# Optimization experiments

Hardware: AMD Instinct MI355X
Metric: run time of the kernel (lower is better)

## Reference

```python
import jax, jax.numpy as jnp
import numpy as np


def _conv1x1(x, w, b):
    # x: [B,C,H,W], w: [O,C], b: [O] -> [B,O,H,W]
    return jnp.einsum('bchw,oc->bohw', x, w) + b[None, :, None, None]


def setup_inputs() -> dict:
    key = jax.random.key(0)
    ks = jax.random.split(key, 11)
    B, C, Ci, H, W = 4, 256, 128, 64, 64
    s_in = 1.0 / np.sqrt(C)
    s_ci = 1.0 / np.sqrt(Ci)
    return {
        'x': jax.random.normal(ks[0], (B, C, H, W), jnp.float32),
        'g_w': jax.random.normal(ks[1], (Ci, C), jnp.float32) * s_in,
        'g_b': jax.random.normal(ks[2], (Ci,), jnp.float32) * 0.01,
        'theta_w': jax.random.normal(ks[3], (Ci, C), jnp.float32) * s_in,
        'theta_b': jax.random.normal(ks[4], (Ci,), jnp.float32) * 0.01,
        'phi_w': jax.random.normal(ks[5], (Ci, C), jnp.float32) * s_in,
        'phi_b': jax.random.normal(ks[6], (Ci,), jnp.float32) * 0.01,
        'wz_w': jax.random.normal(ks[7], (C, Ci), jnp.float32) * s_ci,
        'wz_b': jax.random.normal(ks[8], (C,), jnp.float32) * 0.01,
        'bn_gamma': jax.random.uniform(ks[9], (C,), jnp.float32, 0.5, 1.5),
        'bn_beta': jax.random.normal(ks[10], (C,), jnp.float32) * 0.01,
    }


def reference(x, g_w, g_b, theta_w, theta_b, phi_w, phi_b, wz_w, wz_b, bn_gamma, bn_beta):
    B, C, H, W = x.shape
    Ci = g_w.shape[0]
    N = H * W
    # 1x1 conv projections, flattened over spatial positions
    g_x = _conv1x1(x, g_w, g_b).reshape(B, Ci, N).transpose(0, 2, 1)       # [B,N,Ci]
    theta_x = _conv1x1(x, theta_w, theta_b).reshape(B, Ci, N)              # [B,Ci,N]
    phi_x = _conv1x1(x, phi_w, phi_b).reshape(B, Ci, N)                    # [B,Ci,N]
    # f[b, i, j] = theta_i . phi_j  -> [B,N,N]
    f = jnp.einsum('bci,bcj->bij', theta_x, phi_x)
    # NOTE: softmax over dim=1 (query axis) — faithful to original (non-standard)
    f_div_C = jax.nn.softmax(f, axis=1)
    y = jnp.einsum('bij,bjc->bic', f_div_C, g_x)                           # [B,N,Ci]
    y = y.transpose(0, 2, 1).reshape(B, Ci, H, W)                          # [B,Ci,H,W]
    # W_z: 1x1 conv + BatchNorm2d (training-mode batch statistics)
    w_y = _conv1x1(y, wz_w, wz_b)                                          # [B,C,H,W]
    mean = jnp.mean(w_y, axis=(0, 2, 3), keepdims=True)
    var = jnp.var(w_y, axis=(0, 2, 3), keepdims=True)
    w_y = (w_y - mean) * jax.lax.rsqrt(var + 1e-5)
    w_y = w_y * bn_gamma[None, :, None, None] + bn_beta[None, :, None, None]
    return w_y + x
```

## Files before the change

### kernel.cpp

```cpp
#include <hip/hip_runtime.h>


#define B_  4
#define C_  256
#define CI  128
#define N_  4096
#define NB  (B_*N_)
#define ISPLIT 16
#define MB_ (1u<<20)
#define LOG2E 1.442695041f

typedef _Float16 f16;
typedef f16   f16x8 __attribute__((ext_vector_type(8)));
typedef f16   f16x4 __attribute__((ext_vector_type(4)));
typedef float f32x4 __attribute__((ext_vector_type(4)));
typedef float f32x16 __attribute__((ext_vector_type(16)));
typedef unsigned u32x2 __attribute__((ext_vector_type(2)));
typedef unsigned u32x4v __attribute__((ext_vector_type(4)));

#define MFMA(a,b,c)   __builtin_amdgcn_mfma_f32_16x16x32_f16(a,b,c,0,0,0)
#define MFMA32(a,b,c) __builtin_amdgcn_mfma_f32_32x32x16_f16(a,b,c,0,0,0)

#define GLD16(g, lp) __builtin_amdgcn_global_load_lds( \
    (const __attribute__((address_space(1))) void*)(g), \
    (__attribute__((address_space(3))) void*)(lp), 16, 0, 0)

#define OFF_THETA  0
#define OFF_PHI    (4u*MB_)
#define OFF_G      (8u*MB_)
#define OFF_YP     (12u*MB_)
#define OFF_WY     0
#define OFF_PS     (28u*MB_)
#define OFF_PSUM   OFF_PS
#define OFF_WCVT   (OFF_PS + ISPLIT*NB*4)
#define PSZ ((size_t)B_*N_*CI)

__global__ void k_init(const float* gw, const float* tw, const float* pw,
                       const float* zw, f16* wcvt) {
    int i = blockIdx.x * 256 + threadIdx.x;
    const float* s;
    int which = i >> 15;
    if (which == 0) s = gw; else if (which == 1) s = tw;
    else if (which == 2) s = pw; else s = zw;
    wcvt[i] = (f16)s[i & 32767];
}

__global__ __launch_bounds__(256) void k_proj(
        const float* __restrict__ x, const f16* __restrict__ wcvt,
        const float* __restrict__ gb, const float* __restrict__ tb,
        const float* __restrict__ pb,
        f16* __restrict__ thetaT, f16* __restrict__ phiT, f16* __restrict__ gC) {
    __shared__ __align__(16) f16 xT[32 * 264];
    int bb = blockIdx.x >> 7;
    int n0 = (blockIdx.x & 127) * 32;
    int t = threadIdx.x;

    const float* xb = x + (size_t)bb * C_ * N_;
    for (int rep = 0; rep < 8; rep++) {
        int lin = rep * 256 + t;
        int c = lin >> 3, np = (lin & 7) * 4;
        float4 v = *reinterpret_cast<const float4*>(xb + c * N_ + n0 + np);
        xT[(np + 0) * 264 + c] = (f16)v.x;
        xT[(np + 1) * 264 + c] = (f16)v.y;
        xT[(np + 2) * 264 + c] = (f16)v.z;
        xT[(np + 3) * 264 + c] = (f16)v.w;
    }
    __syncthreads();

    int w = t >> 6, l16 = t & 15, q = (t & 63) >> 4;
    int ci0 = w * 32;
    for (int proj = 0; proj < 3; proj++) {
        const f16* W0 = wcvt + proj * 32768;
        f32x4 acc[2][2] = {};
        for (int kk = 0; kk < 8; kk++) {
            f16x8 a0 = *reinterpret_cast<const f16x8*>(W0 + (ci0 + l16) * 256 + kk * 32 + q * 8);
            f16x8 a1 = *reinterpret_cast<const f16x8*>(W0 + (ci0 + 16 + l16) * 256 + kk * 32 + q * 8);
#pragma unroll
            for (int nt = 0; nt < 2; nt++) {
                f16x8 bv = *reinterpret_cast<const f16x8*>(&xT[(nt * 16 + l16) * 264 + kk * 32 + q * 8]);
                acc[0][nt] = MFMA(a0, bv, acc[0][nt]);
                acc[1][nt] = MFMA(a1, bv, acc[1][nt]);
            }
        }
        const float* bias = (proj == 0) ? gb : (proj == 1) ? tb : pb;
        float scl = (proj == 1) ? LOG2E : 1.0f;
#pragma unroll
        for (int a = 0; a < 2; a++) {
#pragma unroll
            for (int nt = 0; nt < 2; nt++) {
                int n = n0 + nt * 16 + l16;
                int cib = ci0 + a * 16 + q * 4;
                if (proj == 0) {
#pragma unroll
                    for (int r = 0; r < 4; r++)
                        gC[((size_t)bb * CI + cib + r) * N_ + n] = (f16)(acc[a][nt][r] + bias[cib + r]);
                } else {
                    f16x4 v4;
#pragma unroll
                    for (int r = 0; r < 4; r++)
                        v4[r] = (f16)((acc[a][nt][r] + bias[cib + r]) * scl);
                    f16* dst = (proj == 1 ? thetaT : phiT) + ((size_t)bb * N_ + n) * CI + cib;
                    *reinterpret_cast<f16x4*>(dst) = v4;
                }
            }
        }
    }
}

__global__ __launch_bounds__(256, 4) void k_cols(
        const f16* __restrict__ thetaT, const f16* __restrict__ phiT,
        float* __restrict__ ps) {
    __shared__ __align__(16) f16 thS[2][64 * 128];
    int id = blockIdx.x;
    int isp = id & 15, jb = (id >> 4) & 31, bb = id >> 9;
    int t = threadIdx.x, w = t >> 6, l = t & 63;
    int l31 = l & 31, hi = l >> 5;
    int jw = jb * 128 + w * 32 + l31;

    f16x8 pf[8];
    const f16* pb = phiT + ((size_t)bb * N_ + jw) * CI + hi * 8;
#pragma unroll
    for (int kk = 0; kk < 8; kk++)
        pf[kk] = *reinterpret_cast<const f16x8*>(pb + kk * 16);

    const f16* thB = thetaT + ((size_t)bb * N_ + isp * 256) * CI;
    auto stage = [&](int bf, int it0) {
#pragma unroll
        for (int r = 0; r < 4; r++) {
            int p = r * 256 + w * 64 + l;
            int pi = p >> 4, pu = (p & 15) ^ (pi & 15);
            const char* ga = (const char*)(thB + (size_t)(it0 + pi) * CI) + pu * 16;
            GLD16(ga, &thS[bf][(r * 256 + w * 64) * 8]);
        }
    };

    float s = 0.f;
    stage(0, 0);
    __syncthreads();
    for (int it = 0; it < 4; it++) {
        int bf = it & 1;
        if (it + 1 < 4) stage(bf ^ 1, (it + 1) * 64);
#pragma unroll
        for (int it2 = 0; it2 < 2; it2++) {
            f16x8 av[8];
#pragma unroll
            for (int kk = 0; kk < 8; kk++)
                av[kk] = *reinterpret_cast<const f16x8*>(
                    &thS[bf][(it2 * 32 + l31) * 128 + (((kk * 2 + hi) ^ (l31 & 15)) * 8)]);
            f32x16 f = {};
            __builtin_amdgcn_s_setprio(1);
#pragma unroll
            for (int kk = 0; kk < 8; kk++)
                f = MFMA32(av[kk], pf[kk], f);
            __builtin_amdgcn_s_setprio(0);
#pragma unroll
            for (int r = 0; r < 16; r++)
                s += __builtin_amdgcn_exp2f(f[r]);
        }
        __syncthreads();
    }
    s += __shfl_xor(s, 32);
    if (hi == 0)
        ps[isp * NB + bb * N_ + jw] = s;
}

__global__ __launch_bounds__(512, 2) void k_attn(
        const f16* __restrict__ thetaT, const f16* __restrict__ phiT,
        const f16* __restrict__ gC, const float* __restrict__ ps,
        f16* __restrict__ yP) {
    __shared__ __align__(16) char smem[102400];
    f16 (*phiS)[64 * 128] = (f16(*)[64 * 128])smem;
    f16 (*gS)[128 * 64]   = (f16(*)[128 * 64])(smem + 49152);
    float* mdL = (float*)(smem + 98304);

    int jq = blockIdx.x & 3;
    int ib = blockIdx.x >> 2;
    int bb = ib >> 4;
    int i0 = (ib & 15) * 256;
    int t = threadIdx.x, w = t >> 6, l = t & 63;
    int l31 = l & 31, hi = l >> 5;
    int js = w >> 2, iw = w & 3;
    int jbase = jq * 1024;

    {
        const float* pp = ps + bb * N_ + jbase;
        float s0 = 0.f, s1 = 0.f;
#pragma unroll
        for (int isp = 0; isp < ISPLIT; isp++) {
            s0 += pp[isp * NB + t];
            s1 += pp[isp * NB + t + 512];
        }
        mdL[t]       = -__log2f(s0);
        mdL[t + 512] = -__log2f(s1);
    }

    f16x8 ta[2][8];
#pragma unroll
    for (int is = 0; is < 2; is++) {
        const f16* tb = thetaT + ((size_t)bb * N_ + i0 + iw * 64 + is * 32 + l31) * CI + hi * 8;
#pragma unroll
        for (int kk = 0; kk < 8; kk++)
            ta[is][kk] = *reinterpret_cast<const f16x8*>(tb + kk * 16);
    }

    const f16* phiB = phiT + (size_t)bb * N_ * CI;
    const f16* gB   = gC   + (size_t)bb * CI * N_;

    auto stage = [&](int bf, int j0g) {
#pragma unroll
        for (int r = 0; r < 2; r++) {
            int p = r * 512 + t;
            int ub = (r * 512 + w * 64) * 8;
            int pj = p >> 4, pu = (p & 15) ^ (pj & 15);
            const char* ga = (const char*)(phiB + (size_t)(j0g + pj) * CI) + pu * 16;
            GLD16(ga, &phiS[bf][ub]);
            int pc = p >> 3, pu2 = (p & 7) ^ (pc & 7);
            const char* ga2 = (const char*)(gB + (size_t)pc * N_ + j0g) + pu2 * 16;
            GLD16(ga2, &gS[bf][ub]);
        }
    };

    stage(0, jbase);
    stage(1, jbase + 64);
    asm volatile("s_waitcnt vmcnt(4) lgkmcnt(0)" ::: "memory");
    __builtin_amdgcn_s_barrier();

    f32x16 yacc[2][4] = {};
    for (int jt = 0; jt < 16; jt++) {
        int bf = jt % 3;
        if (jt + 2 < 16) stage((jt + 2) % 3, jbase + (jt + 2) * 64);

        f32x16 facc[2];
#pragma unroll
        for (int c = 0; c < 4; c++) {
            f32x4 v = *reinterpret_cast<const f32x4*>(
                &mdL[jt * 64 + js * 32 + c * 8 + hi * 4]);
            facc[0][c * 4 + 0] = v[0]; facc[0][c * 4 + 1] = v[1];
            facc[0][c * 4 + 2] = v[2]; facc[0][c * 4 + 3] = v[3];
            facc[1][c * 4 + 0] = v[0]; facc[1][c * 4 + 1] = v[1];
            facc[1][c * 4 + 2] = v[2]; facc[1][c * 4 + 3] = v[3];
        }

        __builtin_amdgcn_s_setprio(1);
#pragma unroll
        for (int kk = 0; kk < 8; kk++) {
            f16x8 pv = *reinterpret_cast<const f16x8*>(
                &phiS[bf][(js * 32 + l31) * 128 + (((kk * 2 + hi) ^ (l31 & 15)) * 8)]);
            facc[0] = MFMA32(pv, ta[0][kk], facc[0]);
            facc[1] = MFMA32(pv, ta[1][kk], facc[1]);
        }
        __builtin_amdgcn_s_setprio(0);

#pragma unroll
        for (int ch = 0; ch < 2; ch++) {
            f16x8 wfr[2];
#pragma unroll
            for (int is = 0; is < 2; is++) {
                float e0 = __builtin_amdgcn_exp2f(facc[is][ch * 8 + 0]);
                float e1 = __builtin_amdgcn_exp2f(facc[is][ch * 8 + 1]);
                float e2 = __builtin_amdgcn_exp2f(facc[is][ch * 8 + 2]);
                float e3 = __builtin_amdgcn_exp2f(facc[is][ch * 8 + 3]);
                float e4 = __builtin_amdgcn_exp2f(facc[is][ch * 8 + 4]);
                float e5 = __builtin_amdgcn_exp2f(facc[is][ch * 8 + 5]);
                float e6 = __builtin_amdgcn_exp2f(facc[is][ch * 8 + 6]);
                float e7 = __builtin_amdgcn_exp2f(facc[is][ch * 8 + 7]);
                unsigned p01 = __builtin_bit_cast(unsigned, __builtin_amdgcn_cvt_pkrtz(e0, e1));
                unsigned p23 = __builtin_bit_cast(unsigned, __builtin_amdgcn_cvt_pkrtz(e2, e3));
                unsigned p45 = __builtin_bit_cast(unsigned, __builtin_amdgcn_cvt_pkrtz(e4, e5));
                unsigned p67 = __builtin_bit_cast(unsigned, __builtin_amdgcn_cvt_pkrtz(e6, e7));
                u32x2 s0 = __builtin_amdgcn_permlane32_swap(p01, p45, false, false);
                u32x2 s1 = __builtin_amdgcn_permlane32_swap(p23, p67, false, false);
                u32x4v wu = {s0[0], s1[0], s0[1], s1[1]};
                wfr[is] = __builtin_bit_cast(f16x8, wu);
            }
            int jc = js * 2 + ch;
            __builtin_amdgcn_s_setprio(1);
#pragma unroll
            for (int cs = 0; cs < 4; cs++) {
                f16x8 gv = *reinterpret_cast<const f16x8*>(
                    &gS[bf][(cs * 32 + l31) * 64 + (((jc * 2 + hi) ^ (l31 & 7)) * 8)]);
                yacc[0][cs] = MFMA32(wfr[0], gv, yacc[0][cs]);
                yacc[1][cs] = MFMA32(wfr[1], gv, yacc[1][cs]);
            }
            __builtin_amdgcn_s_setprio(0);
        }

        if (jt < 14) { asm volatile("s_waitcnt vmcnt(4)" ::: "memory"); }
        else         { asm volatile("s_waitcnt vmcnt(0)" ::: "memory"); }
        __builtin_amdgcn_s_barrier();
    }

    float* red = (float*)smem;
#pragma unroll
    for (int is = 0; is < 2; is++) {
        __syncthreads();
        if (js == 1) {
#pragma unroll
            for (int cs = 0; cs < 4; cs++)
#pragma unroll
                for (int rq = 0; rq < 4; rq++) {
                    f32x4 v;
                    v[0] = yacc[is][cs][rq * 4 + 0];
                    v[1] = yacc[is][cs][rq * 4 + 1];
                    v[2] = yacc[is][cs][rq * 4 + 2];
                    v[3] = yacc[is][cs][rq * 4 + 3];
                    *reinterpret_cast<f32x4*>(&red[((iw * 4 + cs) * 4 + rq) * 256 + l * 4]) = v;
                }
        }
        __syncthreads();
        if (js == 0) {
#pragma unroll
            for (int cs = 0; cs < 4; cs++)
#pragma unroll
                for (int rq = 0; rq < 4; rq++) {
                    f32x4 v = *reinterpret_cast<const f32x4*>(
                        &red[((iw * 4 + cs) * 4 + rq) * 256 + l * 4]);
                    yacc[is][cs][rq * 4 + 0] += v[0];
                    yacc[is][cs][rq * 4 + 1] += v[1];
                    yacc[is][cs][rq * 4 + 2] += v[2];
                    yacc[is][cs][rq * 4 + 3] += v[3];
                }
        }
    }
    __syncthreads();

    if (js == 0) {
        f16* yw = (f16*)smem + iw * (32 * 136);
#pragma unroll
        for (int is = 0; is < 2; is++) {
#pragma unroll
            for (int cs = 0; cs < 4; cs++)
#pragma unroll
                for (int r = 0; r < 16; r++)
                    yw[((r & 3) + 8 * (r >> 2) + 4 * hi) * 136 + cs * 32 + l31] =
                        (f16)yacc[is][cs][r];
            f16* yo = yP + (size_t)jq * PSZ + ((size_t)bb * N_ + i0 + iw * 64 + is * 32) * CI;
            __builtin_amdgcn_s_waitcnt(0);
#pragma unroll
            for (int rr = 0; rr < 8; rr++) {
                int chunk = rr * 64 + l;
                int il = chunk >> 4, u = chunk & 15;
                *reinterpret_cast<f16x8*>(yo + il * CI + u * 8) =
                    *reinterpret_cast<const f16x8*>(&yw[il * 136 + u * 8]);
            }
            __builtin_amdgcn_s_waitcnt(0);
        }
    }
}

__global__ __launch_bounds__(256) void k_wz(
        const f16* __restrict__ wzc, const f16* __restrict__ yP,
        const float* __restrict__ zb, f16* __restrict__ wy,
        float* __restrict__ psum) {
    int id = blockIdx.x;
    int nb = id & 127, bb = id >> 7;
    int t = threadIdx.x, w = t >> 6, l16 = t & 15, q = (t & 63) >> 4;
    int o0 = w * 64, n0 = nb * 32;
    f32x4 acc[4][2] = {};
#pragma unroll
    for (int kk = 0; kk < 4; kk++) {
        f16x8 bv[2];
#pragma unroll
        for (int nt = 0; nt < 2; nt++) {
            size_t yi = ((size_t)bb * N_ + n0 + nt * 16 + l16) * CI + kk * 32 + q * 8;
            f16x8 b0 = *reinterpret_cast<const f16x8*>(yP + yi);
            f16x8 b1 = *reinterpret_cast<const f16x8*>(yP + PSZ + yi);
            f16x8 b2 = *reinterpret_cast<const f16x8*>(yP + 2 * PSZ + yi);
            f16x8 b3 = *reinterpret_cast<const f16x8*>(yP + 3 * PSZ + yi);
            bv[nt] = (b0 + b1) + (b2 + b3);
        }
#pragma unroll
        for (int os = 0; os < 4; os++) {
            f16x8 av = *reinterpret_cast<const f16x8*>(
                wzc + (o0 + os * 16 + l16) * CI + kk * 32 + q * 8);
#pragma unroll
            for (int nt = 0; nt < 2; nt++)
                acc[os][nt] = MFMA(av, bv[nt], acc[os][nt]);
        }
    }
#pragma unroll
    for (int os = 0; os < 4; os++)
#pragma unroll
    for (int r = 0; r < 4; r++) {
        int o = o0 + os * 16 + q * 4 + r;
        float bias = zb[o];
        float sr = 0.f, qr = 0.f;
#pragma unroll
        for (int nt = 0; nt < 2; nt++) {
            float v = acc[os][nt][r] + bias;
            wy[((size_t)bb * C_ + o) * N_ + n0 + nt * 16 + l16] = (f16)v;
            sr += v; qr += v * v;
        }
#pragma unroll
        for (int off = 1; off < 16; off <<= 1) {
            sr += __shfl_xor(sr, off);
            qr += __shfl_xor(qr, off);
        }
        if (l16 == 0) {
            psum[(o * 2 + 0) * 512 + id] = sr;
            psum[(o * 2 + 1) * 512 + id] = qr;
        }
    }
}

__global__ void k_final(const f16* __restrict__ wy, const float* __restrict__ x,
                        const float* __restrict__ psum,
                        const float* __restrict__ gamma, const float* __restrict__ beta,
                        float* __restrict__ out) {
    __shared__ float s8[8];
    int t = threadIdx.x;
    int p = blockIdx.x * 256 + t;
    int c = (p >> 9) & 255;
    float sr = psum[(c * 2 + 0) * 512 + t] + psum[(c * 2 + 0) * 512 + 256 + t];
    float qr = psum[(c * 2 + 1) * 512 + t] + psum[(c * 2 + 1) * 512 + 256 + t];
#pragma unroll
    for (int off = 1; off < 64; off <<= 1) {
        sr += __shfl_xor(sr, off);
        qr += __shfl_xor(qr, off);
    }
    int w = t >> 6;
    if ((t & 63) == 0) { s8[w * 2] = sr; s8[w * 2 + 1] = qr; }
    __syncthreads();
    float ssum = s8[0] + s8[2] + s8[4] + s8[6];
    float ssq  = s8[1] + s8[3] + s8[5] + s8[7];

    const float inv = 1.0f / 16384.0f;
    float mean = ssum * inv;
    float var = ssq * inv - mean * mean;
    float s = gamma[c] * rsqrtf(var + 1e-5f);
    float h = beta[c] - mean * s;
    f16x8 wv = reinterpret_cast<const f16x8*>(wy)[p];
    float4 x0 = reinterpret_cast<const float4*>(x)[2 * p];
    float4 x1 = reinterpret_cast<const float4*>(x)[2 * p + 1];
    float4 o0, o1;
    o0.x = (float)wv[0] * s + h + x0.x;
    o0.y = (float)wv[1] * s + h + x0.y;
    o0.z = (float)wv[2] * s + h + x0.z;
    o0.w = (float)wv[3] * s + h + x0.w;
    o1.x = (float)wv[4] * s + h + x1.x;
    o1.y = (float)wv[5] * s + h + x1.y;
    o1.z = (float)wv[6] * s + h + x1.z;
    o1.w = (float)wv[7] * s + h + x1.w;
    reinterpret_cast<float4*>(out)[2 * p] = o0;
    reinterpret_cast<float4*>(out)[2 * p + 1] = o1;
}

extern "C" void kernel_launch(void* const* d_in, const int* in_sizes, int n_in,
                              void* d_out, int out_size, void* d_ws, size_t ws_size,
                              hipStream_t stream) {
    const float* x     = (const float*)d_in[0];
    const float* gw    = (const float*)d_in[1];
    const float* gb    = (const float*)d_in[2];
    const float* tw    = (const float*)d_in[3];
    const float* tbv   = (const float*)d_in[4];
    const float* pw    = (const float*)d_in[5];
    const float* pb    = (const float*)d_in[6];
    const float* zw    = (const float*)d_in[7];
    const float* zb    = (const float*)d_in[8];
    const float* gamma = (const float*)d_in[9];
    const float* beta  = (const float*)d_in[10];

    char* ws = (char*)d_ws;
    f16* thetaT = (f16*)(ws + OFF_THETA);
    f16* phiT   = (f16*)(ws + OFF_PHI);
    f16* gC     = (f16*)(ws + OFF_G);
    f16* yP     = (f16*)(ws + OFF_YP);
    f16* wy     = (f16*)(ws + OFF_WY);
    f16* wcvt   = (f16*)(ws + OFF_WCVT);
    float* ps   = (float*)(ws + OFF_PS);
    float* psum = (float*)(ws + OFF_PSUM);

    k_init<<<512, 256, 0, stream>>>(gw, tw, pw, zw, wcvt);
    k_proj<<<512, 256, 0, stream>>>(x, wcvt, gb, tbv, pb, thetaT, phiT, gC);
    k_cols<<<2048, 256, 0, stream>>>(thetaT, phiT, ps);
    k_attn<<<256, 512, 0, stream>>>(thetaT, phiT, gC, ps, yP);
    k_wz<<<512, 256, 0, stream>>>(wcvt + 3 * 32768, yP, zb, wy, psum);
    k_final<<<2048, 256, 0, stream>>>(wy, x, psum, gamma, beta, (float*)d_out);
}
```

Baseline: 188.0 us.

## Fuse all six stages into one cooperative persistent kernel with grid syncs

Replaces the six separate kernel launches with one cooperative kernel of 256 blocks of 512 threads, which uses grid.sync between the weight conversion, projection, column-sum, attention, Wz and BatchNorm-final phases. Each block takes on two or more of the old blocks' work units per phase. The aim is to remove launch gaps and inter-kernel drain and fill overhead. In exchange, phases that previously used 2048 small blocks now run on a fixed grid with serial repetitions, and each grid barrier costs some time.

```diff
diff --git a/kernel.cpp b/kernel.cpp
--- a/kernel.cpp
+++ b/kernel.cpp
@@ -1,5 +1,8 @@
 #include <hip/hip_runtime.h>
-
+#include <hip/hip_cooperative_groups.h>
+
+
+namespace cg = cooperative_groups;
 
 #define B_  4
 #define C_  256
@@ -35,414 +38,437 @@
 #define OFF_WCVT   (OFF_PS + ISPLIT*NB*4)
 #define PSZ ((size_t)B_*N_*CI)
 
-__global__ void k_init(const float* gw, const float* tw, const float* pw,
-                       const float* zw, f16* wcvt) {
-    int i = blockIdx.x * 256 + threadIdx.x;
-    const float* s;
-    int which = i >> 15;
-    if (which == 0) s = gw; else if (which == 1) s = tw;
-    else if (which == 2) s = pw; else s = zw;
-    wcvt[i] = (f16)s[i & 32767];
-}
-
-__global__ __launch_bounds__(256) void k_proj(
-        const float* __restrict__ x, const f16* __restrict__ wcvt,
-        const float* __restrict__ gb, const float* __restrict__ tb,
-        const float* __restrict__ pb,
-        f16* __restrict__ thetaT, f16* __restrict__ phiT, f16* __restrict__ gC) {
-    __shared__ __align__(16) f16 xT[32 * 264];
-    int bb = blockIdx.x >> 7;
-    int n0 = (blockIdx.x & 127) * 32;
+__global__ __launch_bounds__(512, 2) void k_mono(
+        const float* __restrict__ x,
+        const float* __restrict__ gw, const float* __restrict__ gb,
+        const float* __restrict__ tw, const float* __restrict__ tbv,
+        const float* __restrict__ pw, const float* __restrict__ pb,
+        const float* __restrict__ zw, const float* __restrict__ zb,
+        const float* __restrict__ gamma, const float* __restrict__ beta,
+        float* __restrict__ out, char* __restrict__ ws) {
+    cg::grid_group grid = cg::this_grid();
+    __shared__ __align__(16) char smem[102400];
+
+    f16* thetaT = (f16*)(ws + OFF_THETA);
+    f16* phiT   = (f16*)(ws + OFF_PHI);
+    f16* gC     = (f16*)(ws + OFF_G);
+    f16* yP     = (f16*)(ws + OFF_YP);
+    f16* wy     = (f16*)(ws + OFF_WY);
+    f16* wcvt   = (f16*)(ws + OFF_WCVT);
+    float* ps   = (float*)(ws + OFF_PS);
+    float* psum = (float*)(ws + OFF_PSUM);
+
     int t = threadIdx.x;
-
-    const float* xb = x + (size_t)bb * C_ * N_;
-    for (int rep = 0; rep < 8; rep++) {
-        int lin = rep * 256 + t;
-        int c = lin >> 3, np = (lin & 7) * 4;
-        float4 v = *reinterpret_cast<const float4*>(xb + c * N_ + n0 + np);
-        xT[(np + 0) * 264 + c] = (f16)v.x;
-        xT[(np + 1) * 264 + c] = (f16)v.y;
-        xT[(np + 2) * 264 + c] = (f16)v.z;
-        xT[(np + 3) * 264 + c] = (f16)v.w;
-    }
-    __syncthreads();
-
-    int w = t >> 6, l16 = t & 15, q = (t & 63) >> 4;
-    int ci0 = w * 32;
-    for (int proj = 0; proj < 3; proj++) {
-        const f16* W0 = wcvt + proj * 32768;
-        f32x4 acc[2][2] = {};
-        for (int kk = 0; kk < 8; kk++) {
-            f16x8 a0 = *reinterpret_cast<const f16x8*>(W0 + (ci0 + l16) * 256 + kk * 32 + q * 8);
-            f16x8 a1 = *reinterpret_cast<const f16x8*>(W0 + (ci0 + 16 + l16) * 256 + kk * 32 + q * 8);
+    int blk = blockIdx.x;
+    int sub = t >> 8, tt = t & 255;
+
+    {
+        int i = blk * 512 + t;
+        const float* s;
+        int which = i >> 15;
+        if (which == 0) s = gw; else if (which == 1) s = tw;
+        else if (which == 2) s = pw; else s = zw;
+        wcvt[i] = (f16)s[i & 32767];
+    }
+    __threadfence();
+    grid.sync();
+
+    {
+        f16* xT = (f16*)smem + (size_t)sub * (32 * 264);
+        int vid = blk * 2 + sub;
+        int bb = vid >> 7;
+        int n0 = (vid & 127) * 32;
+
+        const float* xb = x + (size_t)bb * C_ * N_;
+        for (int rep = 0; rep < 8; rep++) {
+            int lin = rep * 256 + tt;
+            int c = lin >> 3, np = (lin & 7) * 4;
+            float4 v = *reinterpret_cast<const float4*>(xb + c * N_ + n0 + np);
+            xT[(np + 0) * 264 + c] = (f16)v.x;
+            xT[(np + 1) * 264 + c] = (f16)v.y;
+            xT[(np + 2) * 264 + c] = (f16)v.z;
+            xT[(np + 3) * 264 + c] = (f16)v.w;
+        }
+        __syncthreads();
+
+        int w4 = tt >> 6, l16 = tt & 15, q = (tt & 63) >> 4;
+        int ci0 = w4 * 32;
+        for (int proj = 0; proj < 3; proj++) {
+            const f16* W0 = wcvt + proj * 32768;
+            f32x4 acc[2][2] = {};
+            for (int kk = 0; kk < 8; kk++) {
+                f16x8 a0 = *reinterpret_cast<const f16x8*>(W0 + (ci0 + l16) * 256 + kk * 32 + q * 8);
+                f16x8 a1 = *reinterpret_cast<const f16x8*>(W0 + (ci0 + 16 + l16) * 256 + kk * 32 + q * 8);
+#pragma unroll
+                for (int nt = 0; nt < 2; nt++) {
+                    f16x8 bv = *reinterpret_cast<const f16x8*>(&xT[(nt * 16 + l16) * 264 + kk * 32 + q * 8]);
+                    acc[0][nt] = MFMA(a0, bv, acc[0][nt]);
+                    acc[1][nt] = MFMA(a1, bv, acc[1][nt]);
+                }
+            }
+            const float* bias = (proj == 0) ? gb : (proj == 1) ? tbv : pb;
+            float scl = (proj == 1) ? LOG2E : 1.0f;
+#pragma unroll
+            for (int a = 0; a < 2; a++) {
+#pragma unroll
+                for (int nt = 0; nt < 2; nt++) {
+                    int n = n0 + nt * 16 + l16;
+                    int cib = ci0 + a * 16 + q * 4;
+                    if (proj == 0) {
+#pragma unroll
+                        for (int r = 0; r < 4; r++)
+                            gC[((size_t)bb * CI + cib + r) * N_ + n] = (f16)(acc[a][nt][r] + bias[cib + r]);
+                    } else {
+                        f16x4 v4;
+#pragma unroll
+                        for (int r = 0; r < 4; r++)
+                            v4[r] = (f16)((acc[a][nt][r] + bias[cib + r]) * scl);
+                        f16* dst = (proj == 1 ? thetaT : phiT) + ((size_t)bb * N_ + n) * CI + cib;
+                        *reinterpret_cast<f16x4*>(dst) = v4;
+                    }
+                }
+            }
+        }
+    }
+    __threadfence();
+    grid.sync();
+
+    {
+        f16* thS = (f16*)smem + (size_t)sub * 16384;
+        int wl = tt >> 6, l = tt & 63, l31 = l & 31, hi = l >> 5;
+        for (int rep = 0; rep < 4; rep++) {
+            int unit = blk * 8 + sub * 4 + rep;
+            int isp = unit & 15, jb = (unit >> 4) & 31, bb = unit >> 9;
+            int jw = jb * 128 + wl * 32 + l31;
+
+            f16x8 pf[8];
+            const f16* pb2 = phiT + ((size_t)bb * N_ + jw) * CI + hi * 8;
+#pragma unroll
+            for (int kk = 0; kk < 8; kk++)
+                pf[kk] = *reinterpret_cast<const f16x8*>(pb2 + kk * 16);
+
+            const f16* thB = thetaT + ((size_t)bb * N_ + isp * 256) * CI;
+            auto stage = [&](int bf, int it0) {
+#pragma unroll
+                for (int r = 0; r < 4; r++) {
+                    int p = r * 256 + wl * 64 + l;
+                    int pi = p >> 4, pu = (p & 15) ^ (pi & 15);
+                    const char* ga = (const char*)(thB + (size_t)(it0 + pi) * CI) + pu * 16;
+                    GLD16(ga, thS + bf * 8192 + (r * 256 + wl * 64) * 8);
+                }
+            };
+
+            float s = 0.f;
+            stage(0, 0);
+            __syncthreads();
+            for (int it = 0; it < 4; it++) {
+                int bf = it & 1;
+                if (it + 1 < 4) stage(bf ^ 1, (it + 1) * 64);
+#pragma unroll
+                for (int it2 = 0; it2 < 2; it2++) {
+                    f16x8 av[8];
+#pragma unroll
+                    for (int kk = 0; kk < 8; kk++)
+                        av[kk] = *reinterpret_cast<const f16x8*>(
+                            thS + bf * 8192 + (it2 * 32 + l31) * 128 + (((kk * 2 + hi) ^ (l31 & 15)) * 8));
+                    f32x16 f = {};
+                    __builtin_amdgcn_s_setprio(1);
+#pragma unroll
+                    for (int kk = 0; kk < 8; kk++)
+                        f = MFMA32(av[kk], pf[kk], f);
+                    __builtin_amdgcn_s_setprio(0);
+#pragma unroll
+                    for (int r = 0; r < 16; r++)
+                        s += __builtin_amdgcn_exp2f(f[r]);
+                }
+                __syncthreads();
+            }
+            s += __shfl_xor(s, 32);
+            if (hi == 0)
+                ps[isp * NB + bb * N_ + jw] = s;
+        }
+    }
+    __threadfence();
+    grid.sync();
+
+    {
+        f16 (*phiS)[64 * 128] = (f16(*)[64 * 128])smem;
+        f16 (*gS)[128 * 64]   = (f16(*)[128 * 64])(smem + 49152);
+        float* mdL = (float*)(smem + 98304);
+
+        int jq = blk & 3;
+        int ib = blk >> 2;
+        int bb = ib >> 4;
+        int i0 = (ib & 15) * 256;
+        int w = t >> 6, l = t & 63;
+        int l31 = l & 31, hi = l >> 5;
+        int js = w >> 2, iw = w & 3;
+        int jbase = jq * 1024;
+
+        {
+            const float* pp = ps + bb * N_ + jbase;
+            float s0 = 0.f, s1 = 0.f;
+#pragma unroll
+            for (int isp = 0; isp < ISPLIT; isp++) {
+                s0 += pp[isp * NB + t];
+                s1 += pp[isp * NB + t + 512];
+            }
+            mdL[t]       = -__log2f(s0);
+            mdL[t + 512] = -__log2f(s1);
+        }
+
+        f16x8 ta[2][8];
+#pragma unroll
+        for (int is = 0; is < 2; is++) {
+            const f16* tb = thetaT + ((size_t)bb * N_ + i0 + iw * 64 + is * 32 + l31) * CI + hi * 8;
+#pragma unroll
+            for (int kk = 0; kk < 8; kk++)
+                ta[is][kk] = *reinterpret_cast<const f16x8*>(tb + kk * 16);
+        }
+
+        const f16* phiB = phiT + (size_t)bb * N_ * CI;
+        const f16* gB   = gC   + (size_t)bb * CI * N_;
+
+        auto stage = [&](int bf, int j0g) {
+#pragma unroll
+            for (int r = 0; r < 2; r++) {
+                int p = r * 512 + t;
+                int ub = (r * 512 + w * 64) * 8;
+                int pj = p >> 4, pu = (p & 15) ^ (pj & 15);
+                const char* ga = (const char*)(phiB + (size_t)(j0g + pj) * CI) + pu * 16;
+                GLD16(ga, &phiS[bf][ub]);
+                int pc = p >> 3, pu2 = (p & 7) ^ (pc & 7);
+                const char* ga2 = (const char*)(gB + (size_t)pc * N_ + j0g) + pu2 * 16;
+                GLD16(ga2, &gS[bf][ub]);
+            }
+        };
+
+        stage(0, jbase);
+        stage(1, jbase + 64);
+        asm volatile("s_waitcnt vmcnt(4) lgkmcnt(0)" ::: "memory");
+        __builtin_amdgcn_s_barrier();
+
+        f32x16 yacc[2][4] = {};
+        for (int jt = 0; jt < 16; jt++) {
+            int bf = jt % 3;
+            if (jt + 2 < 16) stage((jt + 2) % 3, jbase + (jt + 2) * 64);
+
+            f32x16 facc[2];
+#pragma unroll
+            for (int c = 0; c < 4; c++) {
+                f32x4 v = *reinterpret_cast<const f32x4*>(
+                    &mdL[jt * 64 + js * 32 + c * 8 + hi * 4]);
+                facc[0][c * 4 + 0] = v[0]; facc[0][c * 4 + 1] = v[1];
+                facc[0][c * 4 + 2] = v[2]; facc[0][c * 4 + 3] = v[3];
+                facc[1][c * 4 + 0] = v[0]; facc[1][c * 4 + 1] = v[1];
+                facc[1][c * 4 + 2] = v[2]; facc[1][c * 4 + 3] = v[3];
+            }
+
+            __builtin_amdgcn_s_setprio(1);
+#pragma unroll
+            for (int kk = 0; kk < 8; kk++) {
+                f16x8 pv = *reinterpret_cast<const f16x8*>(
+                    &phiS[bf][(js * 32 + l31) * 128 + (((kk * 2 + hi) ^ (l31 & 15)) * 8)]);
+                facc[0] = MFMA32(pv, ta[0][kk], facc[0]);
+                facc[1] = MFMA32(pv, ta[1][kk], facc[1]);
+            }
+            __builtin_amdgcn_s_setprio(0);
+
+#pragma unroll
+            for (int ch = 0; ch < 2; ch++) {
+                f16x8 wfr[2];
+#pragma unroll
+                for (int is = 0; is < 2; is++) {
+                    float e0 = __builtin_amdgcn_exp2f(facc[is][ch * 8 + 0]);
+                    float e1 = __builtin_amdgcn_exp2f(facc[is][ch * 8 + 1]);
+                    float e2 = __builtin_amdgcn_exp2f(facc[is][ch * 8 + 2]);
+                    float e3 = __builtin_amdgcn_exp2f(facc[is][ch * 8 + 3]);
+                    float e4 = __builtin_amdgcn_exp2f(facc[is][ch * 8 + 4]);
+                    float e5 = __builtin_amdgcn_exp2f(facc[is][ch * 8 + 5]);
+                    float e6 = __builtin_amdgcn_exp2f(facc[is][ch * 8 + 6]);
+                    float e7 = __builtin_amdgcn_exp2f(facc[is][ch * 8 + 7]);
+                    unsigned p01 = __builtin_bit_cast(unsigned, __builtin_amdgcn_cvt_pkrtz(e0, e1));
+                    unsigned p23 = __builtin_bit_cast(unsigned, __builtin_amdgcn_cvt_pkrtz(e2, e3));
+                    unsigned p45 = __builtin_bit_cast(unsigned, __builtin_amdgcn_cvt_pkrtz(e4, e5));
+                    unsigned p67 = __builtin_bit_cast(unsigned, __builtin_amdgcn_cvt_pkrtz(e6, e7));
+                    u32x2 s0 = __builtin_amdgcn_permlane32_swap(p01, p45, false, false);
+                    u32x2 s1 = __builtin_amdgcn_permlane32_swap(p23, p67, false, false);
+                    u32x4v wu = {s0[0], s1[0], s0[1], s1[1]};
+                    wfr[is] = __builtin_bit_cast(f16x8, wu);
+                }
+                int jc = js * 2 + ch;
+                __builtin_amdgcn_s_setprio(1);
+#pragma unroll
+                for (int cs = 0; cs < 4; cs++) {
+                    f16x8 gv = *reinterpret_cast<const f16x8*>(
+                        &gS[bf][(cs * 32 + l31) * 64 + (((jc * 2 + hi) ^ (l31 & 7)) * 8)]);
+                    yacc[0][cs] = MFMA32(wfr[0], gv, yacc[0][cs]);
+                    yacc[1][cs] = MFMA32(wfr[1], gv, yacc[1][cs]);
+                }
+                __builtin_amdgcn_s_setprio(0);
+            }
+
+            if (jt < 14) { asm volatile("s_waitcnt vmcnt(4)" ::: "memory"); }
+            else         { asm volatile("s_waitcnt vmcnt(0)" ::: "memory"); }
+            __builtin_amdgcn_s_barrier();
+        }
+
+        float* red = (float*)smem;
+#pragma unroll
+        for (int is = 0; is < 2; is++) {
+            __syncthreads();
+            if (js == 1) {
+#pragma unroll
+                for (int cs = 0; cs < 4; cs++)
+#pragma unroll
+                    for (int rq = 0; rq < 4; rq++) {
+                        f32x4 v;
+                        v[0] = yacc[is][cs][rq * 4 + 0];
+                        v[1] = yacc[is][cs][rq * 4 + 1];
+                        v[2] = yacc[is][cs][rq * 4 + 2];
+                        v[3] = yacc[is][cs][rq * 4 + 3];
+                        *reinterpret_cast<f32x4*>(&red[((iw * 4 + cs) * 4 + rq) * 256 + l * 4]) = v;
+                    }
+            }
+            __syncthreads();
+            if (js == 0) {
+#pragma unroll
+                for (int cs = 0; cs < 4; cs++)
+#pragma unroll
+                    for (int rq = 0; rq < 4; rq++) {
+                        f32x4 v = *reinterpret_cast<const f32x4*>(
+                            &red[((iw * 4 + cs) * 4 + rq) * 256 + l * 4]);
+                        yacc[is][cs][rq * 4 + 0] += v[0];
+                        yacc[is][cs][rq * 4 + 1] += v[1];
+                        yacc[is][cs][rq * 4 + 2] += v[2];
+                        yacc[is][cs][rq * 4 + 3] += v[3];
+                    }
+            }
+        }
+        __syncthreads();
+
+        if (js == 0) {
+            f16* yw = (f16*)smem + iw * (32 * 136);
+#pragma unroll
+            for (int is = 0; is < 2; is++) {
+#pragma unroll
+                for (int cs = 0; cs < 4; cs++)
+#pragma unroll
+                    for (int r = 0; r < 16; r++)
+                        yw[((r & 3) + 8 * (r >> 2) + 4 * hi) * 136 + cs * 32 + l31] =
+                            (f16)yacc[is][cs][r];
+                f16* yo = yP + (size_t)jq * PSZ + ((size_t)bb * N_ + i0 + iw * 64 + is * 32) * CI;
+                __builtin_amdgcn_s_waitcnt(0);
+#pragma unroll
+                for (int rr = 0; rr < 8; rr++) {
+                    int chunk = rr * 64 + l;
+                    int il = chunk >> 4, u = chunk & 15;
+                    *reinterpret_cast<f16x8*>(yo + il * CI + u * 8) =
+                        *reinterpret_cast<const f16x8*>(&yw[il * 136 + u * 8]);
+                }
+                __builtin_amdgcn_s_waitcnt(0);
+            }
+        }
+    }
+    __threadfence();
+    grid.sync();
+
+    {
+        const f16* wzc = wcvt + 3 * 32768;
+        int id = blk * 2 + sub;
+        int nb = id & 127, bb = id >> 7;
+        int w4 = tt >> 6, l16 = tt & 15, q = (tt & 63) >> 4;
+        int o0 = w4 * 64, n0 = nb * 32;
+        f32x4 acc[4][2] = {};
+#pragma unroll
+        for (int kk = 0; kk < 4; kk++) {
+            f16x8 bv[2];
 #pragma unroll
             for (int nt = 0; nt < 2; nt++) {
-                f16x8 bv = *reinterpret_cast<const f16x8*>(&xT[(nt * 16 + l16) * 264 + kk * 32 + q * 8]);
-                acc[0][nt] = MFMA(a0, bv, acc[0][nt]);
-                acc[1][nt] = MFMA(a1, bv, acc[1][nt]);
-            }
-        }
-        const float* bias = (proj == 0) ? gb : (proj == 1) ? tb : pb;
-        float scl = (proj == 1) ? LOG2E : 1.0f;
-#pragma unroll
-        for (int a = 0; a < 2; a++) {
+                size_t yi = ((size_t)bb * N_ + n0 + nt * 16 + l16) * CI + kk * 32 + q * 8;
+                f16x8 b0 = *reinterpret_cast<const f16x8*>(yP + yi);
+                f16x8 b1 = *reinterpret_cast<const f16x8*>(yP + PSZ + yi);
+                f16x8 b2 = *reinterpret_cast<const f16x8*>(yP + 2 * PSZ + yi);
+                f16x8 b3 = *reinterpret_cast<const f16x8*>(yP + 3 * PSZ + yi);
+                bv[nt] = (b0 + b1) + (b2 + b3);
+            }
+#pragma unroll
+            for (int os = 0; os < 4; os++) {
+                f16x8 av = *reinterpret_cast<const f16x8*>(
+                    wzc + (o0 + os * 16 + l16) * CI + kk * 32 + q * 8);
+#pragma unroll
+                for (int nt = 0; nt < 2; nt++)
+                    acc[os][nt] = MFMA(av, bv[nt], acc[os][nt]);
+            }
+        }
+#pragma unroll
+        for (int os = 0; os < 4; os++)
+#pragma unroll
+        for (int r = 0; r < 4; r++) {
+            int o = o0 + os * 16 + q * 4 + r;
+            float bias = zb[o];
+            float sr = 0.f, qr = 0.f;
 #pragma unroll
             for (int nt = 0; nt < 2; nt++) {
-                int n = n0 + nt * 16 + l16;
-                int cib = ci0 + a * 16 + q * 4;
-                if (proj == 0) {
-#pragma unroll
-                    for (int r = 0; r < 4; r++)
-                        gC[((size_t)bb * CI + cib + r) * N_ + n] = (f16)(acc[a][nt][r] + bias[cib + r]);
-                } else {
-                    f16x4 v4;
-#pragma unroll
-                    for (int r = 0; r < 4; r++)
-                        v4[r] = (f16)((acc[a][nt][r] + bias[cib + r]) * scl);
-                    f16* dst = (proj == 1 ? thetaT : phiT) + ((size_t)bb * N_ + n) * CI + cib;
-                    *reinterpret_cast<f16x4*>(dst) = v4;
-                }
-            }
-        }
-    }
-}
-
-__global__ __launch_bounds__(256, 4) void k_cols(
-        const f16* __restrict__ thetaT, const f16* __restrict__ phiT,
-        float* __restrict__ ps) {
-    __shared__ __align__(16) f16 thS[2][64 * 128];
-    int id = blockIdx.x;
-    int isp = id & 15, jb = (id >> 4) & 31, bb = id >> 9;
-    int t = threadIdx.x, w = t >> 6, l = t & 63;
-    int l31 = l & 31, hi = l >> 5;
-    int jw = jb * 128 + w * 32 + l31;
-
-    f16x8 pf[8];
-    const f16* pb = phiT + ((size_t)bb * N_ + jw) * CI + hi * 8;
-#pragma unroll
-    for (int kk = 0; kk < 8; kk++)
-        pf[kk] = *reinterpret_cast<const f16x8*>(pb + kk * 16);
-
-    const f16* thB = thetaT + ((size_t)bb * N_ + isp * 256) * CI;
-    auto stage = [&](int bf, int it0) {
-#pragma unroll
-        for (int r = 0; r < 4; r++) {
-            int p = r * 256 + w * 64 + l;
-            int pi = p >> 4, pu = (p & 15) ^ (pi & 15);
-            const char* ga = (const char*)(thB + (size_t)(it0 + pi) * CI) + pu * 16;
-            GLD16(ga, &thS[bf][(r * 256 + w * 64) * 8]);
-        }
-    };
-
-    float s = 0.f;
-    stage(0, 0);
-    __syncthreads();
-    for (int it = 0; it < 4; it++) {
-        int bf = it & 1;
-        if (it + 1 < 4) stage(bf ^ 1, (it + 1) * 64);
-#pragma unroll
-        for (int it2 = 0; it2 < 2; it2++) {
-            f16x8 av[8];
-#pragma unroll
-            for (int kk = 0; kk < 8; kk++)
-                av[kk] = *reinterpret_cast<const f16x8*>(
-                    &thS[bf][(it2 * 32 + l31) * 128 + (((kk * 2 + hi) ^ (l31 & 15)) * 8)]);
-            f32x16 f = {};
-            __builtin_amdgcn_s_setprio(1);
-#pragma unroll
-            for (int kk = 0; kk < 8; kk++)
-                f = MFMA32(av[kk], pf[kk], f);
-            __builtin_amdgcn_s_setprio(0);
-#pragma unroll
-            for (int r = 0; r < 16; r++)
-                s += __builtin_amdgcn_exp2f(f[r]);
-        }
-        __syncthreads();
-    }
-    s += __shfl_xor(s, 32);
-    if (hi == 0)
-        ps[isp * NB + bb * N_ + jw] = s;
-}
-
-__global__ __launch_bounds__(512, 2) void k_attn(
-        const f16* __restrict__ thetaT, const f16* __restrict__ phiT,
-        const f16* __restrict__ gC, const float* __restrict__ ps,
-        f16* __restrict__ yP) {
-    __shared__ __align__(16) char smem[102400];
-    f16 (*phiS)[64 * 128] = (f16(*)[64 * 128])smem;
-    f16 (*gS)[128 * 64]   = (f16(*)[128 * 64])(smem + 49152);
-    float* mdL = (float*)(smem + 98304);
-
-    int jq = blockIdx.x & 3;
-    int ib = blockIdx.x >> 2;
-    int bb = ib >> 4;
-    int i0 = (ib & 15) * 256;
-    int t = threadIdx.x, w = t >> 6, l = t & 63;
-    int l31 = l & 31, hi = l >> 5;
-    int js = w >> 2, iw = w & 3;
-    int jbase = jq * 1024;
-
-    {
-        const float* pp = ps + bb * N_ + jbase;
-        float s0 = 0.f, s1 = 0.f;
-#pragma unroll
-        for (int isp = 0; isp < ISPLIT; isp++) {
-            s0 += pp[isp * NB + t];
-            s1 += pp[isp * NB + t + 512];
-        }
-        mdL[t]       = -__log2f(s0);
-        mdL[t + 512] = -__log2f(s1);
-    }
-
-    f16x8 ta[2][8];
-#pragma unroll
-    for (int is = 0; is < 2; is++) {
-        const f16* tb = thetaT + ((size_t)bb * N_ + i0 + iw * 64 + is * 32 + l31) * CI + hi * 8;
-#pragma unroll
-        for (int kk = 0; kk < 8; kk++)
-            ta[is][kk] = *reinterpret_cast<const f16x8*>(tb + kk * 16);
-    }
-
-    const f16* phiB = phiT + (size_t)bb * N_ * CI;
-    const f16* gB   = gC   + (size_t)bb * CI * N_;
-
-    auto stage = [&](int bf, int j0g) {
-#pragma unroll
-        for (int r = 0; r < 2; r++) {
-            int p = r * 512 + t;
-            int ub = (r * 512 + w * 64) * 8;
-            int pj = p >> 4, pu = (p & 15) ^ (pj & 15);
-            const char* ga = (const char*)(phiB + (size_t)(j0g + pj) * CI) + pu * 16;
-            GLD16(ga, &phiS[bf][ub]);
-            int pc = p >> 3, pu2 = (p & 7) ^ (pc & 7);
-            const char* ga2 = (const char*)(gB + (size_t)pc * N_ + j0g) + pu2 * 16;
-            GLD16(ga2, &gS[bf][ub]);
-        }
-    };
-
-    stage(0, jbase);
-    stage(1, jbase + 64);
-    asm volatile("s_waitcnt vmcnt(4) lgkmcnt(0)" ::: "memory");
-    __builtin_amdgcn_s_barrier();
-
-    f32x16 yacc[2][4] = {};
-    for (int jt = 0; jt < 16; jt++) {
-        int bf = jt % 3;
-        if (jt + 2 < 16) stage((jt + 2) % 3, jbase + (jt + 2) * 64);
-
-        f32x16 facc[2];
-#pragma unroll
-        for (int c = 0; c < 4; c++) {
-            f32x4 v = *reinterpret_cast<const f32x4*>(
-                &mdL[jt * 64 + js * 32 + c * 8 + hi * 4]);
-            facc[0][c * 4 + 0] = v[0]; facc[0][c * 4 + 1] = v[1];
-            facc[0][c * 4 + 2] = v[2]; facc[0][c * 4 + 3] = v[3];
-            facc[1][c * 4 + 0] = v[0]; facc[1][c * 4 + 1] = v[1];
-            facc[1][c * 4 + 2] = v[2]; facc[1][c * 4 + 3] = v[3];
-        }
-
-        __builtin_amdgcn_s_setprio(1);
-#pragma unroll
-        for (int kk = 0; kk < 8; kk++) {
-            f16x8 pv = *reinterpret_cast<const f16x8*>(
-                &phiS[bf][(js * 32 + l31) * 128 + (((kk * 2 + hi) ^ (l31 & 15)) * 8)]);
-            facc[0] = MFMA32(pv, ta[0][kk], facc[0]);
-            facc[1] = MFMA32(pv, ta[1][kk], facc[1]);
-        }
-        __builtin_amdgcn_s_setprio(0);
-
-#pragma unroll
-        for (int ch = 0; ch < 2; ch++) {
-            f16x8 wfr[2];
-#pragma unroll
-            for (int is = 0; is < 2; is++) {
-                float e0 = __builtin_amdgcn_exp2f(facc[is][ch * 8 + 0]);
-                float e1 = __builtin_amdgcn_exp2f(facc[is][ch * 8 + 1]);
-                float e2 = __builtin_amdgcn_exp2f(facc[is][ch * 8 + 2]);
-                float e3 = __builtin_amdgcn_exp2f(facc[is][ch * 8 + 3]);
-                float e4 = __builtin_amdgcn_exp2f(facc[is][ch * 8 + 4]);
-                float e5 = __builtin_amdgcn_exp2f(facc[is][ch * 8 + 5]);
-                float e6 = __builtin_amdgcn_exp2f(facc[is][ch * 8 + 6]);
-                float e7 = __builtin_amdgcn_exp2f(facc[is][ch * 8 + 7]);
-                unsigned p01 = __builtin_bit_cast(unsigned, __builtin_amdgcn_cvt_pkrtz(e0, e1));
-                unsigned p23 = __builtin_bit_cast(unsigned, __builtin_amdgcn_cvt_pkrtz(e2, e3));
-                unsigned p45 = __builtin_bit_cast(unsigned, __builtin_amdgcn_cvt_pkrtz(e4, e5));
-                unsigned p67 = __builtin_bit_cast(unsigned, __builtin_amdgcn_cvt_pkrtz(e6, e7));
-                u32x2 s0 = __builtin_amdgcn_permlane32_swap(p01, p45, false, false);
-                u32x2 s1 = __builtin_amdgcn_permlane32_swap(p23, p67, false, false);
-                u32x4v wu = {s0[0], s1[0], s0[1], s1[1]};
-                wfr[is] = __builtin_bit_cast(f16x8, wu);
-            }
-            int jc = js * 2 + ch;
-            __builtin_amdgcn_s_setprio(1);
-#pragma unroll
-            for (int cs = 0; cs < 4; cs++) {
-                f16x8 gv = *reinterpret_cast<const f16x8*>(
-                    &gS[bf][(cs * 32 + l31) * 64 + (((jc * 2 + hi) ^ (l31 & 7)) * 8)]);
-                yacc[0][cs] = MFMA32(wfr[0], gv, yacc[0][cs]);
-                yacc[1][cs] = MFMA32(wfr[1], gv, yacc[1][cs]);
-            }
-            __builtin_amdgcn_s_setprio(0);
-        }
-
-        if (jt < 14) { asm volatile("s_waitcnt vmcnt(4)" ::: "memory"); }
-        else         { asm volatile("s_waitcnt vmcnt(0)" ::: "memory"); }
-        __builtin_amdgcn_s_barrier();
-    }
-
-    float* red = (float*)smem;
-#pragma unroll
-    for (int is = 0; is < 2; is++) {
-        __syncthreads();
-        if (js == 1) {
-#pragma unroll
-            for (int cs = 0; cs < 4; cs++)
-#pragma unroll
-                for (int rq = 0; rq < 4; rq++) {
-                    f32x4 v;
-                    v[0] = yacc[is][cs][rq * 4 + 0];
-                    v[1] = yacc[is][cs][rq * 4 + 1];
-                    v[2] = yacc[is][cs][rq * 4 + 2];
-                    v[3] = yacc[is][cs][rq * 4 + 3];
-                    *reinterpret_cast<f32x4*>(&red[((iw * 4 + cs) * 4 + rq) * 256 + l * 4]) = v;
-                }
-        }
-        __syncthreads();
-        if (js == 0) {
-#pragma unroll
-            for (int cs = 0; cs < 4; cs++)
-#pragma unroll
-                for (int rq = 0; rq < 4; rq++) {
-                    f32x4 v = *reinterpret_cast<const f32x4*>(
-                        &red[((iw * 4 + cs) * 4 + rq) * 256 + l * 4]);
-                    yacc[is][cs][rq * 4 + 0] += v[0];
-                    yacc[is][cs][rq * 4 + 1] += v[1];
-                    yacc[is][cs][rq * 4 + 2] += v[2];
-                    yacc[is][cs][rq * 4 + 3] += v[3];
-                }
-        }
-    }
-    __syncthreads();
-
-    if (js == 0) {
-        f16* yw = (f16*)smem + iw * (32 * 136);
-#pragma unroll
-        for (int is = 0; is < 2; is++) {
-#pragma unroll
-            for (int cs = 0; cs < 4; cs++)
-#pragma unroll
-                for (int r = 0; r < 16; r++)
-                    yw[((r & 3) + 8 * (r >> 2) + 4 * hi) * 136 + cs * 32 + l31] =
-                        (f16)yacc[is][cs][r];
-            f16* yo = yP + (size_t)jq * PSZ + ((size_t)bb * N_ + i0 + iw * 64 + is * 32) * CI;
-            __builtin_amdgcn_s_waitcnt(0);
-#pragma unroll
-            for (int rr = 0; rr < 8; rr++) {
-                int chunk = rr * 64 + l;
-                int il = chunk >> 4, u = chunk & 15;
-                *reinterpret_cast<f16x8*>(yo + il * CI + u * 8) =
-                    *reinterpret_cast<const f16x8*>(&yw[il * 136 + u * 8]);
-            }
-            __builtin_amdgcn_s_waitcnt(0);
-        }
-    }
-}
-
-__global__ __launch_bounds__(256) void k_wz(
-        const f16* __restrict__ wzc, const f16* __restrict__ yP,
-        const float* __restrict__ zb, f16* __restrict__ wy,
-        float* __restrict__ psum) {
-    int id = blockIdx.x;
-    int nb = id & 127, bb = id >> 7;
-    int t = threadIdx.x, w = t >> 6, l16 = t & 15, q = (t & 63) >> 4;
-    int o0 = w * 64, n0 = nb * 32;
-    f32x4 acc[4][2] = {};
-#pragma unroll
-    for (int kk = 0; kk < 4; kk++) {
-        f16x8 bv[2];
-#pragma unroll
-        for (int nt = 0; nt < 2; nt++) {
-            size_t yi = ((size_t)bb * N_ + n0 + nt * 16 + l16) * CI + kk * 32 + q * 8;
-            f16x8 b0 = *reinterpret_cast<const f16x8*>(yP + yi);
-            f16x8 b1 = *reinterpret_cast<const f16x8*>(yP + PSZ + yi);
-            f16x8 b2 = *reinterpret_cast<const f16x8*>(yP + 2 * PSZ + yi);
-            f16x8 b3 = *reinterpret_cast<const f16x8*>(yP + 3 * PSZ + yi);
-            bv[nt] = (b0 + b1) + (b2 + b3);
-        }
-#pragma unroll
-        for (int os = 0; os < 4; os++) {
-            f16x8 av = *reinterpret_cast<const f16x8*>(
-                wzc + (o0 + os * 16 + l16) * CI + kk * 32 + q * 8);
-#pragma unroll
-            for (int nt = 0; nt < 2; nt++)
-                acc[os][nt] = MFMA(av, bv[nt], acc[os][nt]);
-        }
-    }
-#pragma unroll
-    for (int os = 0; os < 4; os++)
-#pragma unroll
-    for (int r = 0; r < 4; r++) {
-        int o = o0 + os * 16 + q * 4 + r;
-        float bias = zb[o];
-        float sr = 0.f, qr = 0.f;
-#pragma unroll
-        for (int nt = 0; nt < 2; nt++) {
-            float v = acc[os][nt][r] + bias;
-            wy[((size_t)bb * C_ + o) * N_ + n0 + nt * 16 + l16] = (f16)v;
-            sr += v; qr += v * v;
-        }
-#pragma unroll
-        for (int off = 1; off < 16; off <<= 1) {
-            sr += __shfl_xor(sr, off);
-            qr += __shfl_xor(qr, off);
-        }
-        if (l16 == 0) {
-            psum[(o * 2 + 0) * 512 + id] = sr;
-            psum[(o * 2 + 1) * 512 + id] = qr;
-        }
-    }
-}
-
-__global__ void k_final(const f16* __restrict__ wy, const float* __restrict__ x,
-                        const float* __restrict__ psum,
-                        const float* __restrict__ gamma, const float* __restrict__ beta,
-                        float* __restrict__ out) {
-    __shared__ float s8[8];
-    int t = threadIdx.x;
-    int p = blockIdx.x * 256 + t;
-    int c = (p >> 9) & 255;
-    float sr = psum[(c * 2 + 0) * 512 + t] + psum[(c * 2 + 0) * 512 + 256 + t];
-    float qr = psum[(c * 2 + 1) * 512 + t] + psum[(c * 2 + 1) * 512 + 256 + t];
-#pragma unroll
-    for (int off = 1; off < 64; off <<= 1) {
-        sr += __shfl_xor(sr, off);
-        qr += __shfl_xor(qr, off);
-    }
-    int w = t >> 6;
-    if ((t & 63) == 0) { s8[w * 2] = sr; s8[w * 2 + 1] = qr; }
-    __syncthreads();
-    float ssum = s8[0] + s8[2] + s8[4] + s8[6];
-    float ssq  = s8[1] + s8[3] + s8[5] + s8[7];
-
-    const float inv = 1.0f / 16384.0f;
-    float mean = ssum * inv;
-    float var = ssq * inv - mean * mean;
-    float s = gamma[c] * rsqrtf(var + 1e-5f);
-    float h = beta[c] - mean * s;
-    f16x8 wv = reinterpret_cast<const f16x8*>(wy)[p];
-    float4 x0 = reinterpret_cast<const float4*>(x)[2 * p];
-    float4 x1 = reinterpret_cast<const float4*>(x)[2 * p + 1];
-    float4 o0, o1;
-    o0.x = (float)wv[0] * s + h + x0.x;
-    o0.y = (float)wv[1] * s + h + x0.y;
-    o0.z = (float)wv[2] * s + h + x0.z;
-    o0.w = (float)wv[3] * s + h + x0.w;
-    o1.x = (float)wv[4] * s + h + x1.x;
-    o1.y = (float)wv[5] * s + h + x1.y;
-    o1.z = (float)wv[6] * s + h + x1.z;
-    o1.w = (float)wv[7] * s + h + x1.w;
-    reinterpret_cast<float4*>(out)[2 * p] = o0;
-    reinterpret_cast<float4*>(out)[2 * p + 1] = o1;
+                float v = acc[os][nt][r] + bias;
+                wy[((size_t)bb * C_ + o) * N_ + n0 + nt * 16 + l16] = (f16)v;
+                sr += v; qr += v * v;
+            }
+#pragma unroll
+            for (int off = 1; off < 16; off <<= 1) {
+                sr += __shfl_xor(sr, off);
+                qr += __shfl_xor(qr, off);
+            }
+            if (l16 == 0) {
+                psum[(o * 2 + 0) * 512 + id] = sr;
+                psum[(o * 2 + 1) * 512 + id] = qr;
+            }
+        }
+    }
+    __threadfence();
+    grid.sync();
+
+    {
+        float* s8 = (float*)smem + sub * 8;
+        int w4 = tt >> 6;
+        for (int rep = 0; rep < 4; rep++) {
+            int vid = blk * 8 + sub * 4 + rep;
+            int p = vid * 256 + tt;
+            int c = (p >> 9) & 255;
+            float sr = psum[(c * 2 + 0) * 512 + tt] + psum[(c * 2 + 0) * 512 + 256 + tt];
+            float qr = psum[(c * 2 + 1) * 512 + tt] + psum[(c * 2 + 1) * 512 + 256 + tt];
+#pragma unroll
+            for (int off = 1; off < 64; off <<= 1) {
+                sr += __shfl_xor(sr, off);
+                qr += __shfl_xor(qr, off);
+            }
+            if ((tt & 63) == 0) { s8[w4 * 2] = sr; s8[w4 * 2 + 1] = qr; }
+            __syncthreads();
+            float ssum = s8[0] + s8[2] + s8[4] + s8[6];
+            float ssq  = s8[1] + s8[3] + s8[5] + s8[7];
+            __syncthreads();
+
+            const float inv = 1.0f / 16384.0f;
+            float mean = ssum * inv;
+            float var = ssq * inv - mean * mean;
+            float s = gamma[c] * rsqrtf(var + 1e-5f);
+            float h = beta[c] - mean * s;
+            f16x8 wv = reinterpret_cast<const f16x8*>(wy)[p];
+            float4 x0 = reinterpret_cast<const float4*>(x)[2 * p];
+            float4 x1 = reinterpret_cast<const float4*>(x)[2 * p + 1];
+            float4 o0, o1;
+            o0.x = (float)wv[0] * s + h + x0.x;
+            o0.y = (float)wv[1] * s + h + x0.y;
+            o0.z = (float)wv[2] * s + h + x0.z;
+            o0.w = (float)wv[3] * s + h + x0.w;
+            o1.x = (float)wv[4] * s + h + x1.x;
+            o1.y = (float)wv[5] * s + h + x1.y;
+            o1.z = (float)wv[6] * s + h + x1.z;
+            o1.w = (float)wv[7] * s + h + x1.w;
+            reinterpret_cast<float4*>(out)[2 * p] = o0;
+            reinterpret_cast<float4*>(out)[2 * p + 1] = o1;
+        }
+    }
 }
 
 extern "C" void kernel_launch(void* const* d_in, const int* in_sizes, int n_in,
@@ -459,21 +485,12 @@
     const float* zb    = (const float*)d_in[8];
     const float* gamma = (const float*)d_in[9];
     const float* beta  = (const float*)d_in[10];
-
-    char* ws = (char*)d_ws;
-    f16* thetaT = (f16*)(ws + OFF_THETA);
-    f16* phiT   = (f16*)(ws + OFF_PHI);
-    f16* gC     = (f16*)(ws + OFF_G);
-    f16* yP     = (f16*)(ws + OFF_YP);
-    f16* wy     = (f16*)(ws + OFF_WY);
-    f16* wcvt   = (f16*)(ws + OFF_WCVT);
-    float* ps   = (float*)(ws + OFF_PS);
-    float* psum = (float*)(ws + OFF_PSUM);
-
-    k_init<<<512, 256, 0, stream>>>(gw, tw, pw, zw, wcvt);
-    k_proj<<<512, 256, 0, stream>>>(x, wcvt, gb, tbv, pb, thetaT, phiT, gC);
-    k_cols<<<2048, 256, 0, stream>>>(thetaT, phiT, ps);
-    k_attn<<<256, 512, 0, stream>>>(thetaT, phiT, gC, ps, yP);
-    k_wz<<<512, 256, 0, stream>>>(wcvt + 3 * 32768, yP, zb, wy, psum);
-    k_final<<<2048, 256, 0, stream>>>(wy, x, psum, gamma, beta, (float*)d_out);
+    float* outp = (float*)d_out;
+    char* wsp   = (char*)d_ws;
+
+    void* kargs[] = {
+        (void*)&x, (void*)&gw, (void*)&gb, (void*)&tw, (void*)&tbv,
+        (void*)&pw, (void*)&pb, (void*)&zw, (void*)&zb, (void*)&gamma,
+        (void*)&beta, (void*)&outp, (void*)&wsp };
+    hipLaunchCooperativeKernel(k_mono, dim3(256), dim3(512), kargs, 0, stream);
 }
```

Measured after the change: 589.4 us. +213.5%, slower.
